# Kernel tuning notes

Measured on AMD Instinct MI355X. Metric: run time of the kernel, lower is better.

The kernel has to match this reference:

```python
import jax, jax.numpy as jnp
import numpy as np

TAU = 0.1

def setup_inputs() -> dict:
    key = jax.random.key(0)
    kZ, k1, k2 = jax.random.split(key, 3)
    N, D = 8192, 128
    scale = 1.0 / np.sqrt(D)
    return {
        "Z": jax.random.normal(kZ, (N, D), dtype=jnp.float32),
        "W1": jax.random.normal(k1, (D, D), dtype=jnp.float32) * scale,
        "b1": jnp.zeros((D,), dtype=jnp.float32),
        "W2": jax.random.normal(k2, (D, D), dtype=jnp.float32) * scale,
        "b2": jnp.zeros((D,), dtype=jnp.float32),
    }

def reference(Z, W1, b1, W2, b2):
    # DiffusivityTransform: 2-layer MLP with ReLU (torch Linear: x @ W.T + b;
    # here W1/W2 are stored already transposed as [in, out])
    t = jax.nn.relu(Z @ W1 + b1) @ W2 + b2          # [N, D]
    sim = t @ t.T                                     # [N, N]
    S = jax.nn.softmax(sim, axis=1)                   # row-stochastic [N, N]
    Z_prop = S @ Z                                    # [N, D]
    return Z + TAU * (Z_prop - Z)
```

## Files before the change

### kernel.cpp

```cpp
#include <hip/hip_runtime.h>

typedef _Float16 half_t;
typedef _Float16 hx8 __attribute__((ext_vector_type(8)));
typedef _Float16 hx4 __attribute__((ext_vector_type(4)));
typedef float fx4 __attribute__((ext_vector_type(4)));

#define LOG2E 1.44269504088896f
#define TAU 0.1f

__global__ __launch_bounds__(256) void wtrans_kernel(
    const float* __restrict__ W1, const float* __restrict__ W2,
    half_t* __restrict__ W1t, half_t* __restrict__ W2t)
{
  __shared__ float tile[32*132];
  const int bx = blockIdx.x;
  const float* W = (bx & 4) ? W2 : W1;
  half_t* Wt = (bx & 4) ? W2t : W1t;
  const int i0 = (bx & 3) * 32;
  const int tid = threadIdx.x;
  const int r = tid >> 3, cb = tid & 7;
#pragma unroll
  for (int it=0; it<4; ++it) {
    int c4 = cb*4 + it*32;
    *(fx4*)(&tile[r*132 + c4]) = *(const fx4*)(W + (size_t)(i0+r)*128 + c4);
  }
  __syncthreads();
  const int o = tid >> 1, ih = (tid & 1)*16;
  hx8 v0, v1;
#pragma unroll
  for (int u=0;u<8;++u) v0[u] = (half_t)tile[(ih+u)*132 + o];
#pragma unroll
  for (int u=0;u<8;++u) v1[u] = (half_t)tile[(ih+8+u)*132 + o];
  *(hx8*)(Wt + (size_t)o*128 + i0 + ih)     = v0;
  *(hx8*)(Wt + (size_t)o*128 + i0 + ih + 8) = v1;
}

__global__ __launch_bounds__(256) void mlp_kernel(
    const float* __restrict__ Z, const half_t* __restrict__ W1t,
    const float* __restrict__ b1, const half_t* __restrict__ W2t,
    const float* __restrict__ b2, half_t* __restrict__ T)
{
  __shared__ half_t Hs[4][16*136];
  const int tid = threadIdx.x;
  const int w = tid >> 6, lane = tid & 63;
  const int q = lane >> 4, c = lane & 15;
  const int wrow = blockIdx.x*64 + w*16;

  hx8 zb[4];
#pragma unroll
  for (int ks=0;ks<4;++ks) {
    fx4 a = *(const fx4*)(Z + (size_t)(wrow + c)*128 + ks*32 + q*8);
    fx4 b = *(const fx4*)(Z + (size_t)(wrow + c)*128 + ks*32 + q*8 + 4);
#pragma unroll
    for (int u=0;u<4;++u) { zb[ks][u] = (half_t)a[u]; zb[ks][4+u] = (half_t)b[u]; }
  }
  fx4 acc[8];
#pragma unroll
  for (int mt=0;mt<8;++mt) acc[mt] = (fx4){0.f,0.f,0.f,0.f};
#pragma unroll
  for (int mt=0;mt<8;++mt)
#pragma unroll
    for (int ks=0;ks<4;++ks) {
      hx8 aw = *(const hx8*)(W1t + (size_t)(mt*16 + c)*128 + ks*32 + q*8);
      acc[mt] = __builtin_amdgcn_mfma_f32_16x16x32_f16(aw, zb[ks], acc[mt], 0,0,0);
    }
#pragma unroll
  for (int mt=0;mt<8;++mt) {
    fx4 bias = *(const fx4*)(b1 + mt*16 + 4*q);
    hx4 hv;
#pragma unroll
    for (int i=0;i<4;++i) {
      float h = acc[mt][i] + bias[i];
      hv[i] = (half_t)(h > 0.f ? h : 0.f);
    }
    *(hx4*)(&Hs[w][c*136 + mt*16 + 4*q]) = hv;
  }

  hx8 hb[4];
#pragma unroll
  for (int ks=0;ks<4;++ks) hb[ks] = *(const hx8*)(&Hs[w][c*136 + ks*32 + q*8]);
#pragma unroll
  for (int mt=0;mt<8;++mt) acc[mt] = (fx4){0.f,0.f,0.f,0.f};
#pragma unroll
  for (int mt=0;mt<8;++mt)
#pragma unroll
    for (int ks=0;ks<4;++ks) {
      hx8 aw = *(const hx8*)(W2t + (size_t)(mt*16 + c)*128 + ks*32 + q*8);
      acc[mt] = __builtin_amdgcn_mfma_f32_16x16x32_f16(aw, hb[ks], acc[mt], 0,0,0);
    }
#pragma unroll
  for (int mt=0;mt<8;++mt) {
    fx4 bias = *(const fx4*)(b2 + mt*16 + 4*q);
    hx4 tv;
#pragma unroll
    for (int i=0;i<4;++i) tv[i] = (half_t)(acc[mt][i] + bias[i]);
    *(hx4*)(T + (size_t)(wrow + c)*128 + mt*16 + 4*q) = tv;
  }
}

__global__ __launch_bounds__(256) void ztrans_kernel(
    const float* __restrict__ Z, half_t* __restrict__ Zth)
{
  __shared__ float tile[64*36];
  const int tid = threadIdx.x;
  const int nb = blockIdx.x >> 2;
  const int db = blockIdx.x & 3;
#pragma unroll
  for (int i=0;i<2;++i) {
    int fid = i*256 + tid;
    int r = fid >> 3, c4 = (fid & 7) * 4;
    *(fx4*)(&tile[r*36 + c4]) = *(const fx4*)(Z + (size_t)(nb*64 + r)*128 + db*32 + c4);
  }
  __syncthreads();
  const int cr = tid >> 3, j = tid & 7, n0 = j*8;
  hx8 hv;
#pragma unroll
  for (int idx=0;idx<8;++idx) hv[idx] = (half_t)tile[(n0+idx)*36 + cr];
  *(hx8*)(Zth + (size_t)(db*32 + cr)*8192 + nb*64 + n0) = hv;
}

__global__ __launch_bounds__(256,2) void flash_kernel(
    const half_t* __restrict__ T, const half_t* __restrict__ Zt,
    half_t* __restrict__ Pacc, float* __restrict__ Pm, float* __restrict__ Pl)
{
  __shared__ half_t Tks[16*512];
  __shared__ half_t Zts[16*512];
  __shared__ half_t Ps[4][32*72];
  const int tid = threadIdx.x;
  const int w = tid >> 6, lane = tid & 63;
  const int q = lane >> 4, c = lane & 15;
  const int bx = blockIdx.x;
  const int qb = bx >> 3, kh = bx & 7;
  const int wrow = qb*128 + w*32;

  hx8 bq[2][4];
#pragma unroll
  for (int nt=0;nt<2;++nt)
#pragma unroll
    for (int ks=0;ks<4;++ks)
      bq[nt][ks] = *(const hx8*)(T + (size_t)(wrow + nt*16 + c)*128 + ks*32 + q*8);

  fx4 oacc[8][2];
#pragma unroll
  for (int mtd=0;mtd<8;++mtd)
#pragma unroll
    for (int nt=0;nt<2;++nt) oacc[mtd][nt] = (fx4){0.f,0.f,0.f,0.f};
  float m_run[2] = {-1e30f,-1e30f};
  float l_run[2] = {0.f,0.f};

  hx8 pre[8];
  const int kbase = kh*1024;

  auto load_tile = [&](int kt0) {
    if (w < 2) {
#pragma unroll
      for (int i=0;i<8;++i) {
        int f = w*8 + i, mt = f >> 2, ks = f & 3;
        pre[i] = *(const hx8*)(T + (size_t)(kt0 + mt*16 + c)*128 + ks*32 + q*8);
      }
    } else {
#pragma unroll
      for (int i=0;i<8;++i) {
        int f2 = (w-2)*8 + i, mtd = f2 >> 1, ks2 = f2 & 1;
        pre[i] = *(const hx8*)(Zt + (size_t)(mtd*16 + c)*8192 + kt0 + ks2*32 + q*8);
      }
    }
  };
  auto store_tile = [&]() {
    if (w < 2) {
#pragma unroll
      for (int i=0;i<8;++i) { int f = w*8 + i; *(hx8*)(&Tks[f*512 + lane*8]) = pre[i]; }
    } else {
#pragma unroll
      for (int i=0;i<8;++i) { int f2 = (w-2)*8 + i; *(hx8*)(&Zts[f2*512 + lane*8]) = pre[i]; }
    }
  };

  load_tile(kbase);
  for (int t=0;t<16;++t) {
    __syncthreads();
    store_tile();
    __syncthreads();
    if (t < 15) load_tile(kbase + (t+1)*64);

    fx4 sacc[4][2];
#pragma unroll
    for (int mt=0;mt<4;++mt)
#pragma unroll
      for (int nt=0;nt<2;++nt) sacc[mt][nt] = (fx4){0.f,0.f,0.f,0.f};
#pragma unroll
    for (int ks=0;ks<4;++ks)
#pragma unroll
      for (int mt=0;mt<4;++mt) {
        hx8 ak = *(const hx8*)(&Tks[(mt*4+ks)*512 + lane*8]);
        sacc[mt][0] = __builtin_amdgcn_mfma_f32_16x16x32_f16(ak, bq[0][ks], sacc[mt][0], 0,0,0);
        sacc[mt][1] = __builtin_amdgcn_mfma_f32_16x16x32_f16(ak, bq[1][ks], sacc[mt][1], 0,0,0);
      }

#pragma unroll
    for (int nt=0;nt<2;++nt) {
      float mx = -1e30f;
#pragma unroll
      for (int mt=0;mt<4;++mt)
#pragma unroll
        for (int i=0;i<4;++i) mx = fmaxf(mx, sacc[mt][nt][i]);
      mx = fmaxf(mx, __shfl_xor(mx, 16, 64));
      mx = fmaxf(mx, __shfl_xor(mx, 32, 64));
      float mnew = fmaxf(m_run[nt], mx);
      float alpha = __builtin_amdgcn_exp2f((m_run[nt]-mnew)*LOG2E);
      m_run[nt] = mnew;
      float nb = mnew*LOG2E;
      float rs = 0.f;
#pragma unroll
      for (int mt=0;mt<4;++mt) {
        hx4 pk;
#pragma unroll
        for (int i=0;i<4;++i) {
          float p = __builtin_amdgcn_exp2f(sacc[mt][nt][i]*LOG2E - nb);
          rs += p;
          pk[i] = (half_t)p;
        }
        *(hx4*)(&Ps[w][(nt*16 + c)*72 + mt*16 + 4*q]) = pk;
      }
      rs += __shfl_xor(rs, 16, 64);
      rs += __shfl_xor(rs, 32, 64);
      l_run[nt] = l_run[nt]*alpha + rs;
#pragma unroll
      for (int mtd=0;mtd<8;++mtd)
#pragma unroll
        for (int i=0;i<4;++i) oacc[mtd][nt][i] *= alpha;
    }

#pragma unroll
    for (int ks2=0;ks2<2;++ks2) {
      hx8 bp0 = *(const hx8*)(&Ps[w][(c     )*72 + ks2*32 + q*8]);
      hx8 bp1 = *(const hx8*)(&Ps[w][(16 + c)*72 + ks2*32 + q*8]);
#pragma unroll
      for (int mtd=0;mtd<8;++mtd) {
        hx8 az = *(const hx8*)(&Zts[(mtd*2+ks2)*512 + lane*8]);
        oacc[mtd][0] = __builtin_amdgcn_mfma_f32_16x16x32_f16(az, bp0, oacc[mtd][0], 0,0,0);
        oacc[mtd][1] = __builtin_amdgcn_mfma_f32_16x16x32_f16(az, bp1, oacc[mtd][1], 0,0,0);
      }
    }
  }

#pragma unroll
  for (int nt=0;nt<2;++nt) {
    float inv = 1.0f / l_run[nt];
    const size_t rowg = (size_t)(bx*128 + w*32 + nt*16 + c);
#pragma unroll
    for (int mtd=0;mtd<8;++mtd) {
      hx4 ov;
#pragma unroll
      for (int i=0;i<4;++i) ov[i] = (half_t)(oacc[mtd][nt][i]*inv);
      *(hx4*)(Pacc + rowg*128 + mtd*16 + 4*q) = ov;
    }
    if (q == 0) {
      Pm[rowg] = m_run[nt];
      Pl[rowg] = l_run[nt];
    }
  }
}

__global__ __launch_bounds__(256) void merge_kernel(
    const float* __restrict__ Z, const half_t* __restrict__ Pacc,
    const float* __restrict__ Pm, const float* __restrict__ Pl,
    float* __restrict__ out)
{
  const int th = blockIdx.x*256 + threadIdx.x;
  const int r = th >> 5, cg = th & 31;
  const int qb = r >> 7, rr = r & 127;
  float mk[8], lk[8];
  float M = -1e30f;
#pragma unroll
  for (int k=0;k<8;++k) {
    int p = qb*8 + k;
    mk[k] = Pm[p*128 + rr];
    lk[k] = Pl[p*128 + rr];
    M = fmaxf(M, mk[k]);
  }
  float L = 0.f, wk[8];
#pragma unroll
  for (int k=0;k<8;++k) { wk[k] = lk[k]*__builtin_amdgcn_exp2f((mk[k]-M)*LOG2E); L += wk[k]; }
  float o0=0.f,o1=0.f,o2=0.f,o3=0.f;
#pragma unroll
  for (int k=0;k<8;++k) {
    int p = qb*8 + k;
    hx4 v = *(const hx4*)(Pacc + ((size_t)p*128 + rr)*128 + cg*4);
    o0 += wk[k]*(float)v[0]; o1 += wk[k]*(float)v[1];
    o2 += wk[k]*(float)v[2]; o3 += wk[k]*(float)v[3];
  }
  float invL = 1.0f / L;
  fx4 zv = *(const fx4*)(Z + (size_t)r*128 + cg*4);
  fx4 res;
  res[0] = (1.f-TAU)*zv[0] + TAU*o0*invL;
  res[1] = (1.f-TAU)*zv[1] + TAU*o1*invL;
  res[2] = (1.f-TAU)*zv[2] + TAU*o2*invL;
  res[3] = (1.f-TAU)*zv[3] + TAU*o3*invL;
  *(fx4*)(out + (size_t)r*128 + cg*4) = res;
}

extern "C" void kernel_launch(void* const* d_in, const int* in_sizes, int n_in,
                              void* d_out, int out_size, void* d_ws, size_t ws_size,
                              hipStream_t stream) {
  const float* Z  = (const float*)d_in[0];
  const float* W1 = (const float*)d_in[1];
  const float* b1 = (const float*)d_in[2];
  const float* W2 = (const float*)d_in[3];
  const float* b2 = (const float*)d_in[4];
  float* out = (float*)d_out;

  char* ws = (char*)d_ws;
  half_t* Thi  = (half_t*)(ws);
  half_t* Zth  = (half_t*)(ws + (size_t)2*1024*1024);
  half_t* Pacc = (half_t*)(ws + (size_t)4*1024*1024);
  float*  Pm   = (float*)(ws + (size_t)4*1024*1024 + (size_t)512*128*128*2);
  float*  Pl   = Pm + 512*128;
  half_t* W1t  = (half_t*)(ws + (size_t)4*1024*1024 + (size_t)512*128*128*2 + (size_t)2*512*128*4);
  half_t* W2t  = W1t + 128*128;

  hipLaunchKernelGGL(wtrans_kernel, dim3(8),    dim3(256), 0, stream, W1, W2, W1t, W2t);
  hipLaunchKernelGGL(ztrans_kernel, dim3(512),  dim3(256), 0, stream, Z, Zth);
  hipLaunchKernelGGL(mlp_kernel,    dim3(128),  dim3(256), 0, stream, Z, W1t, b1, W2t, b2, Thi);
  hipLaunchKernelGGL(flash_kernel,  dim3(512),  dim3(256), 0, stream, Thi, Zth, Pacc, Pm, Pl);
  hipLaunchKernelGGL(merge_kernel,  dim3(1024), dim3(256), 0, stream, Z, Pacc, Pm, Pl, out);
}
```

Baseline: 138.8 us.

## Double flash key split, merge transpose kernels, shrink MLP blocks

Splits the key dimension of the flash stage into 16 chunks instead of 8, doubling the grid to 1024 blocks, and raises the occupancy hint to 3 blocks per SIMD group. The weight and Z transposes are fused into one prep kernel, saving a launch. The MLP kernel uses 128-thread blocks over twice as many blocks. The aim is to fill more compute units on the MI355X, at the cost of twice the partial-output traffic (Pacc/Pm/Pl) and a heavier merge pass.

```diff
diff --git a/kernel.cpp b/kernel.cpp
--- a/kernel.cpp
+++ b/kernel.cpp
@@ -7,44 +7,66 @@
 
 #define LOG2E 1.44269504088896f
 #define TAU 0.1f
-
-__global__ __launch_bounds__(256) void wtrans_kernel(
+#define NSPLIT 16
+
+__global__ __launch_bounds__(256) void prep_kernel(
     const float* __restrict__ W1, const float* __restrict__ W2,
-    half_t* __restrict__ W1t, half_t* __restrict__ W2t)
+    const float* __restrict__ Z,
+    half_t* __restrict__ W1t, half_t* __restrict__ W2t,
+    half_t* __restrict__ Zth)
 {
   __shared__ float tile[32*132];
   const int bx = blockIdx.x;
-  const float* W = (bx & 4) ? W2 : W1;
-  half_t* Wt = (bx & 4) ? W2t : W1t;
-  const int i0 = (bx & 3) * 32;
   const int tid = threadIdx.x;
-  const int r = tid >> 3, cb = tid & 7;
-#pragma unroll
-  for (int it=0; it<4; ++it) {
-    int c4 = cb*4 + it*32;
-    *(fx4*)(&tile[r*132 + c4]) = *(const fx4*)(W + (size_t)(i0+r)*128 + c4);
-  }
-  __syncthreads();
-  const int o = tid >> 1, ih = (tid & 1)*16;
-  hx8 v0, v1;
-#pragma unroll
-  for (int u=0;u<8;++u) v0[u] = (half_t)tile[(ih+u)*132 + o];
-#pragma unroll
-  for (int u=0;u<8;++u) v1[u] = (half_t)tile[(ih+8+u)*132 + o];
-  *(hx8*)(Wt + (size_t)o*128 + i0 + ih)     = v0;
-  *(hx8*)(Wt + (size_t)o*128 + i0 + ih + 8) = v1;
-}
-
-__global__ __launch_bounds__(256) void mlp_kernel(
+  if (bx < 8) {
+    const float* W = (bx & 4) ? W2 : W1;
+    half_t* Wt = (bx & 4) ? W2t : W1t;
+    const int i0 = (bx & 3) * 32;
+    const int r = tid >> 3, cb = tid & 7;
+#pragma unroll
+    for (int it=0; it<4; ++it) {
+      int c4 = cb*4 + it*32;
+      *(fx4*)(&tile[r*132 + c4]) = *(const fx4*)(W + (size_t)(i0+r)*128 + c4);
+    }
+    __syncthreads();
+    const int o = tid >> 1, ih = (tid & 1)*16;
+    hx8 v0, v1;
+#pragma unroll
+    for (int u=0;u<8;++u) v0[u] = (half_t)tile[(ih+u)*132 + o];
+#pragma unroll
+    for (int u=0;u<8;++u) v1[u] = (half_t)tile[(ih+8+u)*132 + o];
+    *(hx8*)(Wt + (size_t)o*128 + i0 + ih)     = v0;
+    *(hx8*)(Wt + (size_t)o*128 + i0 + ih + 8) = v1;
+  } else {
+    float* zt = tile;
+    const int b = bx - 8;
+    const int nb = b >> 2;
+    const int db = b & 3;
+#pragma unroll
+    for (int i=0;i<2;++i) {
+      int fid = i*256 + tid;
+      int r = fid >> 3, c4 = (fid & 7) * 4;
+      *(fx4*)(&zt[r*36 + c4]) = *(const fx4*)(Z + (size_t)(nb*64 + r)*128 + db*32 + c4);
+    }
+    __syncthreads();
+    const int cr = tid >> 3, j = tid & 7, n0 = j*8;
+    hx8 hv;
+#pragma unroll
+    for (int idx=0;idx<8;++idx) hv[idx] = (half_t)zt[(n0+idx)*36 + cr];
+    *(hx8*)(Zth + (size_t)(db*32 + cr)*8192 + nb*64 + n0) = hv;
+  }
+}
+
+__global__ __launch_bounds__(128) void mlp_kernel(
     const float* __restrict__ Z, const half_t* __restrict__ W1t,
     const float* __restrict__ b1, const half_t* __restrict__ W2t,
     const float* __restrict__ b2, half_t* __restrict__ T)
 {
-  __shared__ half_t Hs[4][16*136];
+  __shared__ half_t Hs[2][16*136];
   const int tid = threadIdx.x;
   const int w = tid >> 6, lane = tid & 63;
   const int q = lane >> 4, c = lane & 15;
-  const int wrow = blockIdx.x*64 + w*16;
+  const int wrow = blockIdx.x*32 + w*16;
 
   hx8 zb[4];
 #pragma unroll
@@ -98,28 +120,7 @@
   }
 }
 
-__global__ __launch_bounds__(256) void ztrans_kernel(
-    const float* __restrict__ Z, half_t* __restrict__ Zth)
-{
-  __shared__ float tile[64*36];
-  const int tid = threadIdx.x;
-  const int nb = blockIdx.x >> 2;
-  const int db = blockIdx.x & 3;
-#pragma unroll
-  for (int i=0;i<2;++i) {
-    int fid = i*256 + tid;
-    int r = fid >> 3, c4 = (fid & 7) * 4;
-    *(fx4*)(&tile[r*36 + c4]) = *(const fx4*)(Z + (size_t)(nb*64 + r)*128 + db*32 + c4);
-  }
-  __syncthreads();
-  const int cr = tid >> 3, j = tid & 7, n0 = j*8;
-  hx8 hv;
-#pragma unroll
-  for (int idx=0;idx<8;++idx) hv[idx] = (half_t)tile[(n0+idx)*36 + cr];
-  *(hx8*)(Zth + (size_t)(db*32 + cr)*8192 + nb*64 + n0) = hv;
-}
-
-__global__ __launch_bounds__(256,2) void flash_kernel(
+__global__ __launch_bounds__(256,3) void flash_kernel(
     const half_t* __restrict__ T, const half_t* __restrict__ Zt,
     half_t* __restrict__ Pacc, float* __restrict__ Pm, float* __restrict__ Pl)
 {
@@ -130,7 +131,7 @@
   const int w = tid >> 6, lane = tid & 63;
   const int q = lane >> 4, c = lane & 15;
   const int bx = blockIdx.x;
-  const int qb = bx >> 3, kh = bx & 7;
+  const int qb = bx >> 4, kh = bx & 15;
   const int wrow = qb*128 + w*32;
 
   hx8 bq[2][4];
@@ -149,7 +150,7 @@
   float l_run[2] = {0.f,0.f};
 
   hx8 pre[8];
-  const int kbase = kh*1024;
+  const int kbase = kh*512;
 
   auto load_tile = [&](int kt0) {
     if (w < 2) {
@@ -177,11 +178,11 @@
   };
 
   load_tile(kbase);
-  for (int t=0;t<16;++t) {
+  for (int t=0;t<8;++t) {
     __syncthreads();
     store_tile();
     __syncthreads();
-    if (t < 15) load_tile(kbase + (t+1)*64);
+    if (t < 7) load_tile(kbase + (t+1)*64);
 
     fx4 sacc[4][2];
 #pragma unroll
@@ -270,22 +271,22 @@
   const int th = blockIdx.x*256 + threadIdx.x;
   const int r = th >> 5, cg = th & 31;
   const int qb = r >> 7, rr = r & 127;
-  float mk[8], lk[8];
+  float mk[NSPLIT], lk[NSPLIT];
   float M = -1e30f;
 #pragma unroll
-  for (int k=0;k<8;++k) {
-    int p = qb*8 + k;
+  for (int k=0;k<NSPLIT;++k) {
+    int p = qb*NSPLIT + k;
     mk[k] = Pm[p*128 + rr];
     lk[k] = Pl[p*128 + rr];
     M = fmaxf(M, mk[k]);
   }
-  float L = 0.f, wk[8];
-#pragma unroll
-  for (int k=0;k<8;++k) { wk[k] = lk[k]*__builtin_amdgcn_exp2f((mk[k]-M)*LOG2E); L += wk[k]; }
+  float L = 0.f, wk[NSPLIT];
+#pragma unroll
+  for (int k=0;k<NSPLIT;++k) { wk[k] = lk[k]*__builtin_amdgcn_exp2f((mk[k]-M)*LOG2E); L += wk[k]; }
   float o0=0.f,o1=0.f,o2=0.f,o3=0.f;
 #pragma unroll
-  for (int k=0;k<8;++k) {
-    int p = qb*8 + k;
+  for (int k=0;k<NSPLIT;++k) {
+    int p = qb*NSPLIT + k;
     hx4 v = *(const hx4*)(Pacc + ((size_t)p*128 + rr)*128 + cg*4);
     o0 += wk[k]*(float)v[0]; o1 += wk[k]*(float)v[1];
     o2 += wk[k]*(float)v[2]; o3 += wk[k]*(float)v[3];
@@ -311,17 +312,17 @@
   float* out = (float*)d_out;
 
   char* ws = (char*)d_ws;
+  const size_t NBLK = 64 * NSPLIT;
   half_t* Thi  = (half_t*)(ws);
   half_t* Zth  = (half_t*)(ws + (size_t)2*1024*1024);
   half_t* Pacc = (half_t*)(ws + (size_t)4*1024*1024);
-  float*  Pm   = (float*)(ws + (size_t)4*1024*1024 + (size_t)512*128*128*2);
-  float*  Pl   = Pm + 512*128;
-  half_t* W1t  = (half_t*)(ws + (size_t)4*1024*1024 + (size_t)512*128*128*2 + (size_t)2*512*128*4);
+  float*  Pm   = (float*)(ws + (size_t)4*1024*1024 + NBLK*128*128*2);
+  float*  Pl   = Pm + NBLK*128;
+  half_t* W1t  = (half_t*)(ws + (size_t)4*1024*1024 + NBLK*128*128*2 + 2*NBLK*128*4);
   half_t* W2t  = W1t + 128*128;
 
-  hipLaunchKernelGGL(wtrans_kernel, dim3(8),    dim3(256), 0, stream, W1, W2, W1t, W2t);
-  hipLaunchKernelGGL(ztrans_kernel, dim3(512),  dim3(256), 0, stream, Z, Zth);
-  hipLaunchKernelGGL(mlp_kernel,    dim3(128),  dim3(256), 0, stream, Z, W1t, b1, W2t, b2, Thi);
-  hipLaunchKernelGGL(flash_kernel,  dim3(512),  dim3(256), 0, stream, Thi, Zth, Pacc, Pm, Pl);
-  hipLaunchKernelGGL(merge_kernel,  dim3(1024), dim3(256), 0, stream, Z, Pacc, Pm, Pl, out);
-}
+  hipLaunchKernelGGL(prep_kernel,  dim3(520),  dim3(256), 0, stream, W1, W2, Z, W1t, W2t, Zth);
+  hipLaunchKernelGGL(mlp_kernel,   dim3(256),  dim3(128), 0, stream, Z, W1t, b1, W2t, b2, Thi);
+  hipLaunchKernelGGL(flash_kernel, dim3(NBLK), dim3(256), 0, stream, Thi, Zth, Pacc, Pm, Pl);
+  hipLaunchKernelGGL(merge_kernel, dim3(1024), dim3(256), 0, stream, Z, Pacc, Pm, Pl, out);
+}
```

New measurement: 211.2 us. 1.52x slower.
